# Kernel optimization log

Measured on AMD Instinct MI355X. Metric: run time of the kernel, lower is better.

Reference implementation:

```python
import jax, jax.numpy as jnp
import numpy as np

B, IN_C, L, D, K, DEPTH, OUT = 16, 3, 2048, 256, 8, 4, 1
F = L // 2 + 1
EPS = 1e-5


def _hilbert_basis_rfft(grid_size, k):
    # Hilbert matrix Z[i,j] = 1/(i+j+1), symmetric PSD; take top-k eigvecs.
    i = np.arange(grid_size, dtype=np.float64)
    Z = 1.0 / (i[:, None] + i[None, :] + 1.0)
    w, V = np.linalg.eigh(Z)
    idx = np.argsort(w)[::-1][:k]
    Vt = V.T[idx]                                   # (k, L)
    Phi_f = np.fft.rfft(Vt, n=grid_size, axis=-1)   # (k, L//2+1) complex
    return Phi_f.astype(np.complex64)


def setup_inputs() -> dict:
    key = jax.random.key(0)
    ks = jax.random.split(key, 10)
    phi = _hilbert_basis_rfft(L, K)
    s = 0.05
    return {
        "x": jax.random.normal(ks[0], (B, IN_C, L), jnp.float32),
        "lift_w": jax.random.normal(ks[1], (D, IN_C + 1), jnp.float32) * s,
        "lift_b": jax.random.normal(ks[2], (D,), jnp.float32) * s,
        "theta": jax.random.normal(ks[3], (DEPTH, K, D, D), jnp.float32) * (1.0 / np.sqrt(D)),
        "ln_gamma": jnp.ones((DEPTH, D), jnp.float32),
        "ln_beta": jnp.zeros((DEPTH, D), jnp.float32),
        "glu_val_w": jax.random.normal(ks[4], (DEPTH, D, D), jnp.float32) * (1.0 / np.sqrt(D)),
        "glu_val_b": jax.random.normal(ks[5], (DEPTH, D), jnp.float32) * s,
        "glu_gate_w": jax.random.normal(ks[6], (DEPTH, D, D), jnp.float32) * (1.0 / np.sqrt(D)),
        "glu_gate_b": jax.random.normal(ks[7], (DEPTH, D), jnp.float32) * s,
        "head_w": jax.random.normal(ks[8], (OUT, D), jnp.float32) * (1.0 / np.sqrt(D)),
        "head_b": jax.random.normal(ks[9], (OUT,), jnp.float32) * s,
        "phi_real": jnp.asarray(phi.real, jnp.float32),
        "phi_imag": jnp.asarray(phi.imag, jnp.float32),
    }


def _layernorm_channels(h, gamma, beta):
    # h: (b, d, t); normalize over channel dim d (matches LayerNorm on transposed input)
    mu = jnp.mean(h, axis=1, keepdims=True)
    var = jnp.mean(jnp.square(h - mu), axis=1, keepdims=True)
    z = (h - mu) * jax.lax.rsqrt(var + EPS)
    return z * gamma[None, :, None] + beta[None, :, None]


def reference(x, lift_w, lift_b, theta, ln_gamma, ln_beta,
              glu_val_w, glu_val_b, glu_gate_w, glu_gate_b,
              head_w, head_b, phi_real, phi_imag):
    phi = phi_real + 1j * phi_imag                      # (K, F) complex
    phi_c = jnp.conj(phi)
    # add grid coordinate channel
    coords = jnp.linspace(0.0, 1.0, L, dtype=x.dtype)
    coords = jnp.broadcast_to(coords[None, None, :], (x.shape[0], 1, L))
    h = jnp.concatenate([x, coords], axis=1)            # (b, in+1, L)
    # pointwise lift (Conv1d kernel_size=1, norm=Identity)
    h = jnp.einsum("oi,bit->bot", lift_w, h) + lift_b[None, :, None]
    for i in range(DEPTH):
        z = _layernorm_channels(h, ln_gamma[i], ln_beta[i])
        Xf = jnp.fft.rfft(z, axis=-1)                   # (b, d, F) complex64
        # Exploit FFT linearity: S = sum_{l,d} Theta[l,h,d] * irfft(Xf[b,d] * conj(Phi[l]))
        #                          = irfft( sum_{l,d} Theta[l,h,d]*conj(Phi[l,f]) * Xf[b,d,f] )
        W = jnp.einsum("lhd,lf->hdf", theta[i].astype(Xf.dtype), phi_c)  # (h, d, F)
        Sf = jnp.einsum("bdf,hdf->bhf", Xf, W)          # (b, h, F)
        S = jnp.fft.irfft(Sf, n=L, axis=-1)             # (b, h, L)
        V = jnp.einsum("od,bdt->bot", glu_val_w[i], S) + glu_val_b[i][None, :, None]
        G = jax.nn.sigmoid(jnp.einsum("od,bdt->bot", glu_gate_w[i], S) + glu_gate_b[i][None, :, None])
        h = h + V * G                                   # residual + GLU
    y = jnp.einsum("od,bdt->bot", head_w, h) + head_b[None, :, None]
    return y
```

## Files before the change

kernel.cpp:

```cpp
#include <hip/hip_runtime.h>
#include <math.h>

#define NB 16
#define CIN 3
#define LL 2048
#define DD 256
#define KK 8
#define NDEPTH 4
#define FF 1025
#define FFP 1032
#define LOGL 11

typedef _Float16 half8 __attribute__((ext_vector_type(8)));
typedef float f32x4 __attribute__((ext_vector_type(4)));

union H8 { half8 h8; unsigned int u[4]; uint4 q; };
union H2 { _Float16 h[2]; unsigned int u; };

__device__ inline float2 cmul(const float2 a, const float2 b){
    return make_float2(a.x*b.x - a.y*b.y, a.x*b.y + a.y*b.x);
}

__global__ void twiddle_kernel(float2* __restrict__ tw){
    int j = blockIdx.x*blockDim.x + threadIdx.x;
    if (j < LL/2){
        double ang = -2.0*3.14159265358979323846*(double)j/(double)LL;
        tw[j] = make_float2((float)cos(ang), (float)sin(ang));
    }
}

__global__ void conv_w_kernel(const float* __restrict__ wv, const float* __restrict__ wg,
                              _Float16* __restrict__ Wf){
    int idx = blockIdx.x*256 + threadIdx.x;
    int layer = idx >> 17;
    int vg = (idx >> 16) & 1;
    int rem = idx & 65535;
    int o = rem >> 8, d = rem & 255;
    const float* src = (vg ? wg : wv) + ((size_t)layer << 16);
    float val = src[(o << 8) + d];
    size_t dst = ((((size_t)(layer*2+vg)*16 + (o>>4))*8 + (d>>5))*64
                  + (o&15) + 16*((d>>3)&3))*8 + (d&7);
    Wf[dst] = (_Float16)val;
}

__global__ void transpose_theta_kernel(const float* __restrict__ in, float* __restrict__ out){
    __shared__ float tile[32][33];
    int m = blockIdx.z;
    int c0 = blockIdx.x*32, r0 = blockIdx.y*32;
    int tx = threadIdx.x & 31, ty = threadIdx.x >> 5;
    const float* src = in + (size_t)m*DD*DD;
    float* dst = out + (size_t)m*DD*DD;
    #pragma unroll
    for (int i = 0; i < 4; ++i){
        tile[ty + i*8][tx] = src[(size_t)(r0 + ty + i*8)*DD + c0 + tx];
    }
    __syncthreads();
    #pragma unroll
    for (int i = 0; i < 4; ++i){
        dst[(size_t)(c0 + ty + i*8)*DD + r0 + tx] = tile[tx][ty + i*8];
    }
}

__global__ __launch_bounds__(256) void lift_ln_kernel(const float* __restrict__ x,
        const float* __restrict__ lw, const float* __restrict__ lb,
        const float* __restrict__ gamma, const float* __restrict__ beta,
        float* __restrict__ h, float* __restrict__ z){
    __shared__ float red[2][4][64];
    __shared__ float stat[2][64];
    __shared__ float gb[512];
    int tid = threadIdx.x;
    int t = tid & 63, dg = tid >> 6;
    int b = blockIdx.y;
    int tg = blockIdx.x*64 + t;
    gb[tid] = gamma[tid];
    gb[256 + tid] = beta[tid];
    const float* xb = x + (size_t)b*CIN*LL;
    float x0 = xb[tg], x1 = xb[LL + tg], x2 = xb[2*LL + tg];
    float coord = (float)tg * (1.0f/(LL-1));
    float hv[64];
    float s = 0.f, ss = 0.f;
    float* hp = h + (size_t)b*DD*LL + tg;
    #pragma unroll
    for (int j = 0; j < 64; ++j){
        int d = dg*64 + j;
        float4 w = *(const float4*)&lw[d*4];
        float v = lb[d];
        v = fmaf(w.x, x0, v); v = fmaf(w.y, x1, v);
        v = fmaf(w.z, x2, v); v = fmaf(w.w, coord, v);
        hv[j] = v;
        s += v; ss = fmaf(v, v, ss);
        hp[(size_t)d*LL] = v;
    }
    red[0][dg][t] = s; red[1][dg][t] = ss;
    __syncthreads();
    if (tid < 64){
        float S1 = red[0][0][tid] + red[0][1][tid] + red[0][2][tid] + red[0][3][tid];
        float S2 = red[1][0][tid] + red[1][1][tid] + red[1][2][tid] + red[1][3][tid];
        float mu = S1*(1.0f/DD);
        float var = S2*(1.0f/DD) - mu*mu;
        stat[0][tid] = mu;
        stat[1][tid] = rsqrtf(var + 1e-5f);
    }
    __syncthreads();
    float mu = stat[0][t], rs = stat[1][t];
    float* zp = z + (size_t)b*DD*LL + tg;
    #pragma unroll
    for (int j = 0; j < 64; ++j){
        int d = dg*64 + j;
        zp[(size_t)d*LL] = (hv[j] - mu)*rs*gb[d] + gb[256 + d];
    }
}

__global__ __launch_bounds__(256) void fft_fwd_pair_kernel(const float* __restrict__ in,
                                                           unsigned int* __restrict__ XfH,
                                                           const float2* __restrict__ tw){
    __shared__ float2 a[LL];
    int blk = blockIdx.x;
    const float* src0 = in + (size_t)(blk*2)*LL;
    const float* src1 = src0 + LL;
    int tid = threadIdx.x;
    #pragma unroll
    for (int i = 0; i < LL/256; ++i){
        int idx = tid + i*256;
        int rev = __brev((unsigned)idx) >> (32-LOGL);
        a[rev] = make_float2(src0[idx], src1[idx]);
    }
    __syncthreads();
    for (int s = 0; s < LOGL; ++s){
        int half = 1 << s;
        #pragma unroll
        for (int jj = 0; jj < 4; ++jj){
            int j = tid + jj*256;
            int grp = j >> s;
            int pos = j & (half-1);
            int i1 = (grp << (s+1)) + pos;
            int i2 = i1 + half;
            float2 w = tw[pos << (LOGL-1-s)];
            float2 u = a[i1];
            float2 v = cmul(w, a[i2]);
            a[i1] = make_float2(u.x+v.x, u.y+v.y);
            a[i2] = make_float2(u.x-v.x, u.y-v.y);
        }
        __syncthreads();
    }
    unsigned int* dst0 = XfH + (size_t)(blk*2)*FFP;
    unsigned int* dst1 = dst0 + FFP;
    #pragma unroll
    for (int i = 0; i < 5; ++i){
        int f = tid + i*256;
        if (f <= 1024){
            int m = (LL - f) & (LL-1);
            float2 A = a[f], B = a[m];
            H2 p0, p1;
            p0.h[0] = (_Float16)(0.5f*(A.x + B.x));
            p0.h[1] = (_Float16)(0.5f*(A.y - B.y));
            p1.h[0] = (_Float16)(0.5f*(A.y + B.y));
            p1.h[1] = (_Float16)(0.5f*(B.x - A.x));
            dst0[f] = p0.u;
            dst1[f] = p1.u;
        }
    }
}

__global__ __launch_bounds__(256) void fft_inv_pair_kernel(const float2* __restrict__ in,
                                                           unsigned int* __restrict__ Sfrag,
                                                           const float2* __restrict__ tw){
    __shared__ float2 a[LL];
    int blk = blockIdx.x;
    const float2* src0 = in + (size_t)(blk*2)*FF;
    const float2* src1 = src0 + FF;
    int tid = threadIdx.x;
    #pragma unroll
    for (int i = 0; i < LL/256; ++i){
        int idx = tid + i*256;
        float2 Y;
        if (idx <= 1024){
            float2 s0 = src0[idx], s1 = src1[idx];
            Y = make_float2(s0.x - s1.y, s0.y + s1.x);
        } else {
            int m = LL - idx;
            float2 s0 = src0[m], s1 = src1[m];
            Y = make_float2(s0.x + s1.y, s1.x - s0.y);
        }
        int rev = __brev((unsigned)idx) >> (32-LOGL);
        a[rev] = Y;
    }
    __syncthreads();
    for (int s = 0; s < LOGL; ++s){
        int half = 1 << s;
        #pragma unroll
        for (int jj = 0; jj < 4; ++jj){
            int j = tid + jj*256;
            int grp = j >> s;
            int pos = j & (half-1);
            int i1 = (grp << (s+1)) + pos;
            int i2 = i1 + half;
            float2 w = tw[pos << (LOGL-1-s)];
            w.y = -w.y;
            float2 u = a[i1];
            float2 v = cmul(w, a[i2]);
            a[i1] = make_float2(u.x+v.x, u.y+v.y);
            a[i2] = make_float2(u.x-v.x, u.y-v.y);
        }
        __syncthreads();
    }
    int b = blk >> 7, dl = (blk & 127)*2;
    int kc = dl >> 5, lq4 = (dl >> 3) & 3, jh = (dl & 7) >> 1;
    unsigned int* dst = Sfrag + ((size_t)(b*8 + kc)*128)*64*4;
    const float sc = 1.0f/(float)LL;
    #pragma unroll
    for (int i = 0; i < LL/256; ++i){
        int t = tid + i*256;
        float2 v = a[t];
        H2 p;
        p.h[0] = (_Float16)(v.x*sc);
        p.h[1] = (_Float16)(v.y*sc);
        dst[(((t>>4)*64) + (t&15) + 16*lq4)*4 + jh] = p.u;
    }
}

__global__ __launch_bounds__(256, 2) void spectral3_kernel(
    const unsigned int* __restrict__ XfH,
    const float* __restrict__ thetaT,
    const float* __restrict__ phr, const float* __restrict__ phim,
    float2* __restrict__ Sf){
    __shared__ unsigned int Apairs[8*64*8];
    __shared__ float2 phi_s[8*KK];
    int tid = threadIdx.x;
    int w = tid >> 6, lane = tid & 63;
    int n = lane & 15, kp = lane >> 4;
    int f0 = blockIdx.x * 8;
    int h0 = blockIdx.y * 64;
    int h = h0 + w*16 + n;

    if (tid < 64){
        int ff = tid >> 3, l = tid & 7;
        phi_s[tid] = make_float2(phr[l*FF + f0 + ff], -phim[l*FF + f0 + ff]);
    }

    f32x4 accre[8], accim[8];
    #pragma unroll
    for (int i = 0; i < 8; ++i){
        accre[i] = (f32x4){0.f,0.f,0.f,0.f};
        accim[i] = (f32x4){0.f,0.f,0.f,0.f};
    }

    for (int kc = 0; kc < 8; ++kc){
        float th[8][8];
        #pragma unroll
        for (int l = 0; l < 8; ++l)
            #pragma unroll
            for (int j = 0; j < 8; ++j)
                th[l][j] = thetaT[((size_t)(l*DD) + kc*32 + kp*8 + j)*DD + h];

        __syncthreads();
        #pragma unroll
        for (int s = 0; s < 2; ++s){
            int b = tid & 15;
            int dd = s*16 + (tid >> 4);
            const uint4* src = (const uint4*)(XfH + ((size_t)(b*DD + kc*32 + dd)*FFP + f0));
            uint4 v0 = src[0], v1 = src[1];
            int L = b + 16*(dd >> 3), j = dd & 7;
            unsigned int vv[8] = {v0.x, v0.y, v0.z, v0.w, v1.x, v1.y, v1.z, v1.w};
            #pragma unroll
            for (int ff = 0; ff < 8; ++ff){
                int A = ff*2048 + L*32 + j*4;
                A ^= ((A >> 7) & 3) << 5;
                *(unsigned int*)((char*)Apairs + A) = vv[ff];
            }
        }
        __syncthreads();

        #pragma unroll
        for (int ff = 0; ff < 8; ++ff){
            float pr[8], pi[8];
            #pragma unroll
            for (int l = 0; l < 8; ++l){
                float2 p = phi_s[ff*8 + l];
                pr[l] = p.x; pi[l] = p.y;
            }
            int Ab = ff*2048 + lane*32;
            Ab ^= ((Ab >> 7) & 3) << 5;
            uint4 lo = *(const uint4*)((const char*)Apairs + Ab);
            uint4 hi = *(const uint4*)((const char*)Apairs + Ab + 16);
            unsigned int dw[8] = {lo.x, lo.y, lo.z, lo.w, hi.x, hi.y, hi.z, hi.w};
            H8 Are, Aim, Anim;
            #pragma unroll
            for (int k = 0; k < 4; ++k){
                Are.u[k]  = __builtin_amdgcn_perm(dw[2*k+1], dw[2*k], 0x05040100u);
                Aim.u[k]  = __builtin_amdgcn_perm(dw[2*k+1], dw[2*k], 0x07060302u);
                Anim.u[k] = Aim.u[k] ^ 0x80008000u;
            }
            float wre[8], wim[8];
            #pragma unroll
            for (int j = 0; j < 8; ++j){
                float re = 0.f, im = 0.f;
                #pragma unroll
                for (int l = 0; l < 8; ++l){
                    re = fmaf(th[l][j], pr[l], re);
                    im = fmaf(th[l][j], pi[l], im);
                }
                wre[j] = re; wim[j] = im;
            }
            H8 Bre, Bim;
            #pragma unroll
            for (int j = 0; j < 8; ++j){
                Bre.h8[j] = (_Float16)wre[j];
                Bim.h8[j] = (_Float16)wim[j];
            }
            accre[ff] = __builtin_amdgcn_mfma_f32_16x16x32_f16(Are.h8,  Bre.h8, accre[ff], 0, 0, 0);
            accre[ff] = __builtin_amdgcn_mfma_f32_16x16x32_f16(Anim.h8, Bim.h8, accre[ff], 0, 0, 0);
            accim[ff] = __builtin_amdgcn_mfma_f32_16x16x32_f16(Are.h8,  Bim.h8, accim[ff], 0, 0, 0);
            accim[ff] = __builtin_amdgcn_mfma_f32_16x16x32_f16(Aim.h8,  Bre.h8, accim[ff], 0, 0, 0);
        }
    }
    #pragma unroll
    for (int ff = 0; ff < 8; ++ff){
        #pragma unroll
        for (int r = 0; r < 4; ++r){
            int b = kp*4 + r;
            Sf[((size_t)(b*DD) + h)*FF + f0 + ff] = make_float2(accre[ff][r], accim[ff][r]);
        }
    }
}

__global__ __launch_bounds__(256) void nyq_kernel(const unsigned int* __restrict__ XfH,
    const float* __restrict__ thetaT,
    const float* __restrict__ phr, const float* __restrict__ phim,
    float2* __restrict__ Sf){
    __shared__ float2 red[256];
    int tid = threadIdx.x;
    int hb = blockIdx.x, b = blockIdx.y;
    int h = hb*16 + (tid & 15);
    int dp = tid >> 4;
    float pr[KK], pi[KK];
    #pragma unroll
    for (int l = 0; l < KK; ++l){ pr[l] = phr[l*FF + 1024]; pi[l] = -phim[l*FF + 1024]; }
    float2 acc = make_float2(0.f, 0.f);
    for (int j = 0; j < 16; ++j){
        int d = dp*16 + j;
        float wre = 0.f, wim = 0.f;
        #pragma unroll
        for (int l = 0; l < KK; ++l){
            float t = thetaT[((size_t)l*DD + d)*DD + h];
            wre = fmaf(t, pr[l], wre);
            wim = fmaf(t, pi[l], wim);
        }
        H2 u; u.u = XfH[(size_t)(b*DD + d)*FFP + 1024];
        float2 x = make_float2((float)u.h[0], (float)u.h[1]);
        acc.x = fmaf(x.x, wre, fmaf(-x.y, wim, acc.x));
        acc.y = fmaf(x.x, wim, fmaf( x.y, wre, acc.y));
    }
    red[tid] = acc;
    __syncthreads();
    if (tid < 16){
        float2 s = make_float2(0.f, 0.f);
        #pragma unroll
        for (int k = 0; k < 16; ++k){ s.x += red[tid + k*16].x; s.y += red[tid + k*16].y; }
        Sf[((size_t)b*DD + hb*16 + tid)*FF + 1024] = s;
    }
}

template<int MODE>
__global__ __launch_bounds__(256, 2) void glu_mfma_kernel(
    const uint4* __restrict__ Sfrag,
    const uint4* __restrict__ WfL,
    const float* __restrict__ bv, const float* __restrict__ bg,
    float* __restrict__ h, float* __restrict__ outp,
    const float* __restrict__ aux1, const float* __restrict__ aux2){
    __shared__ float sb[1024];
    __shared__ float red[2][4][4][16];
    __shared__ float stat[2][4][16];
    int tid = threadIdx.x;
    int w = tid >> 6, lane = tid & 63;
    int tl = lane & 15, lq = lane >> 4;
    int b = blockIdx.y, tb4 = blockIdx.x;

    sb[tid] = bv[tid];
    sb[256 + tid] = bg[tid];
    sb[512 + tid] = aux1[tid];
    if (MODE == 0) sb[768 + tid] = aux2[tid];
    __syncthreads();

    f32x4 aV[4][4], aG[4][4];
    #pragma unroll
    for (int mt = 0; mt < 4; ++mt)
        #pragma unroll
        for (int nt = 0; nt < 4; ++nt){
            aV[mt][nt] = (f32x4){0.f,0.f,0.f,0.f};
            aG[mt][nt] = (f32x4){0.f,0.f,0.f,0.f};
        }

    for (int kc = 0; kc < 8; ++kc){
        H8 Bf[4];
        #pragma unroll
        for (int nt = 0; nt < 4; ++nt)
            Bf[nt].q = Sfrag[((size_t)(b*8 + kc)*128 + tb4*4 + nt)*64 + lane];
        H8 Av[4], Ag[4];
        #pragma unroll
        for (int mt = 0; mt < 4; ++mt){
            int ot = w*4 + mt;
            Av[mt].q = WfL[((size_t)(ot)*8 + kc)*64 + lane];
            Ag[mt].q = WfL[((size_t)(16 + ot)*8 + kc)*64 + lane];
        }
        #pragma unroll
        for (int mt = 0; mt < 4; ++mt)
            #pragma unroll
            for (int nt = 0; nt < 4; ++nt){
                aV[mt][nt] = __builtin_amdgcn_mfma_f32_16x16x32_f16(Av[mt].h8, Bf[nt].h8, aV[mt][nt], 0, 0, 0);
                aG[mt][nt] = __builtin_amdgcn_mfma_f32_16x16x32_f16(Ag[mt].h8, Bf[nt].h8, aG[mt][nt], 0, 0, 0);
            }
    }

    #pragma unroll
    for (int mt = 0; mt < 4; ++mt){
        #pragma unroll
        for (int r = 0; r < 4; ++r){
            int o = w*64 + mt*16 + lq*4 + r;
            float bvv = sb[o], bgv = sb[256 + o];
            float* hp = h + ((size_t)(b*DD + o))*LL + tb4*64 + tl;
            #pragma unroll
            for (int nt = 0; nt < 4; ++nt){
                float v = aV[mt][nt][r] + bvv;
                float g = aG[mt][nt][r] + bgv;
                g = 1.0f/(1.0f + __expf(-g));
                float cur = hp[nt*16] + v*g;
                if (MODE == 0) hp[nt*16] = cur;
                aV[mt][nt][r] = cur;
            }
        }
    }

    float s[4], ss[4];
    #pragma unroll
    for (int nt = 0; nt < 4; ++nt){ s[nt] = 0.f; ss[nt] = 0.f; }
    #pragma unroll
    for (int mt = 0; mt < 4; ++mt)
        #pragma unroll
        for (int r = 0; r < 4; ++r){
            int o = w*64 + mt*16 + lq*4 + r;
            float wo = (MODE == 0) ? 1.0f : sb[512 + o];
            #pragma unroll
            for (int nt = 0; nt < 4; ++nt){
                float cur = aV[mt][nt][r];
                if (MODE == 0){ s[nt] += cur; ss[nt] = fmaf(cur, cur, ss[nt]); }
                else { s[nt] = fmaf(wo, cur, s[nt]); }
            }
        }
    #pragma unroll
    for (int nt = 0; nt < 4; ++nt){
        s[nt] += __shfl_xor(s[nt], 16); s[nt] += __shfl_xor(s[nt], 32);
        if (MODE == 0){ ss[nt] += __shfl_xor(ss[nt], 16); ss[nt] += __shfl_xor(ss[nt], 32); }
    }
    if (lq == 0){
        #pragma unroll
        for (int nt = 0; nt < 4; ++nt){
            red[0][w][nt][tl] = s[nt];
            if (MODE == 0) red[1][w][nt][tl] = ss[nt];
        }
    }
    __syncthreads();
    if (MODE == 0){
        if (tid < 64){
            int nt = tid >> 4, t2 = tid & 15;
            float S1 = red[0][0][nt][t2] + red[0][1][nt][t2] + red[0][2][nt][t2] + red[0][3][nt][t2];
            float S2 = red[1][0][nt][t2] + red[1][1][nt][t2] + red[1][2][nt][t2] + red[1][3][nt][t2];
            float mu = S1*(1.0f/DD);
            float var = S2*(1.0f/DD) - mu*mu;
            stat[0][nt][t2] = mu;
            stat[1][nt][t2] = rsqrtf(var + 1e-5f);
        }
        __syncthreads();
        #pragma unroll
        for (int mt = 0; mt < 4; ++mt){
            #pragma unroll
            for (int r = 0; r < 4; ++r){
                int o = w*64 + mt*16 + lq*4 + r;
                float gam = sb[512 + o], bet = sb[768 + o];
                float* zp = outp + ((size_t)(b*DD + o))*LL + tb4*64 + tl;
                #pragma unroll
                for (int nt = 0; nt < 4; ++nt){
                    float zv = (aV[mt][nt][r] - stat[0][nt][tl])*stat[1][nt][tl]*gam + bet;
                    zp[nt*16] = zv;
                }
            }
        }
    } else {
        if (tid < 64){
            int nt = tid >> 4, t2 = tid & 15;
            float S1 = red[0][0][nt][t2] + red[0][1][nt][t2] + red[0][2][nt][t2] + red[0][3][nt][t2];
            outp[(size_t)b*LL + tb4*64 + tid] = S1 + aux2[0];
        }
    }
}

extern "C" void kernel_launch(void* const* d_in, const int* in_sizes, int n_in,
                              void* d_out, int out_size, void* d_ws, size_t ws_size,
                              hipStream_t stream){
    (void)in_sizes; (void)n_in; (void)out_size; (void)ws_size;
    const float* x      = (const float*)d_in[0];
    const float* lift_w = (const float*)d_in[1];
    const float* lift_b = (const float*)d_in[2];
    const float* theta  = (const float*)d_in[3];
    const float* ln_g   = (const float*)d_in[4];
    const float* ln_b   = (const float*)d_in[5];
    const float* gvw    = (const float*)d_in[6];
    const float* gvb    = (const float*)d_in[7];
    const float* ggw    = (const float*)d_in[8];
    const float* ggb    = (const float*)d_in[9];
    const float* hw     = (const float*)d_in[10];
    const float* hb     = (const float*)d_in[11];
    const float* phr    = (const float*)d_in[12];
    const float* phim   = (const float*)d_in[13];
    float* out = (float*)d_out;

    char* ws = (char*)d_ws;
    size_t off = 0;
    float2* tw  = (float2*)(ws + off); off += (size_t)(LL/2)*sizeof(float2);
    _Float16* Wf = (_Float16*)(ws + off); off += (size_t)NDEPTH*2*DD*DD*2;
    float*  thT = (float*)(ws + off);  off += (size_t)NDEPTH*KK*DD*DD*4;
    off = (off + 255) & ~(size_t)255;
    float*  h   = (float*)(ws + off);  off += (size_t)NB*DD*LL*4;
    float*  z   = (float*)(ws + off);  off += (size_t)NB*DD*LL*4;
    unsigned int* XfH = (unsigned int*)(ws + off); off += (size_t)NB*DD*FFP*4;
    unsigned int* Sfrag = XfH;
    off = (off + 255) & ~(size_t)255;
    float2* Sf  = (float2*)(ws + off); off += (size_t)NB*DD*FF*8;

    twiddle_kernel<<<4, 256, 0, stream>>>(tw);
    conv_w_kernel<<<(NDEPTH*2*DD*DD)/256, 256, 0, stream>>>(gvw, ggw, Wf);
    transpose_theta_kernel<<<dim3(8,8,NDEPTH*KK), 256, 0, stream>>>(theta, thT);
    lift_ln_kernel<<<dim3(LL/64, NB), 256, 0, stream>>>(x, lift_w, lift_b, ln_g, ln_b, h, z);

    for (int layer = 0; layer < NDEPTH; ++layer){
        const float* thL = thT + (size_t)layer*KK*DD*DD;
        const uint4* WfL = (const uint4*)(Wf + (size_t)layer*2*DD*DD);
        fft_fwd_pair_kernel<<<NB*DD/2, 256, 0, stream>>>(z, XfH, tw);
        spectral3_kernel<<<dim3(128,4), 256, 0, stream>>>(XfH, thL, phr, phim, Sf);
        nyq_kernel<<<dim3(16,16), 256, 0, stream>>>(XfH, thL, phr, phim, Sf);
        fft_inv_pair_kernel<<<NB*DD/2, 256, 0, stream>>>(Sf, Sfrag, tw);
        if (layer < NDEPTH-1){
            glu_mfma_kernel<0><<<dim3(LL/64, NB), 256, 0, stream>>>(
                (const uint4*)Sfrag, WfL,
                gvb + layer*DD, ggb + layer*DD, h, z,
                ln_g + (layer+1)*DD, ln_b + (layer+1)*DD);
        } else {
            glu_mfma_kernel<1><<<dim3(LL/64, NB), 256, 0, stream>>>(
                (const uint4*)Sfrag, WfL,
                gvb + layer*DD, ggb + layer*DD, h, out, hw, hb);
        }
    }
}
```

Measured before the change: 604.6 us.

## Use radix-4 FFT stages and split spectral work across more blocks

The forward and inverse FFT kernels now use fused radix-4 passes (five of them) plus one final radix-2 pass, replacing eleven radix-2 passes. This cuts the number of shared-memory round trips and barriers per transform. The spectral kernel now has each wave handle 4 frequencies for 16 output channels instead of 8 frequencies for 64 channels. It launches twice as many blocks with a higher occupancy hint, but the shared A tile and the theta loads are now repeated in more blocks.

```diff
diff --git a/kernel.cpp b/kernel.cpp
--- a/kernel.cpp
+++ b/kernel.cpp
@@ -126,23 +126,43 @@
         a[rev] = make_float2(src0[idx], src1[idx]);
     }
     __syncthreads();
-    for (int s = 0; s < LOGL; ++s){
-        int half = 1 << s;
-        #pragma unroll
-        for (int jj = 0; jj < 4; ++jj){
-            int j = tid + jj*256;
-            int grp = j >> s;
-            int pos = j & (half-1);
-            int i1 = (grp << (s+1)) + pos;
-            int i2 = i1 + half;
-            float2 w = tw[pos << (LOGL-1-s)];
-            float2 u = a[i1];
-            float2 v = cmul(w, a[i2]);
-            a[i1] = make_float2(u.x+v.x, u.y+v.y);
-            a[i2] = make_float2(u.x-v.x, u.y-v.y);
+    #pragma unroll
+    for (int sp = 0; sp < 5; ++sp){
+        const int s = sp*2;
+        const int hs = 1 << s;
+        #pragma unroll
+        for (int gg = 0; gg < 2; ++gg){
+            int g = tid + gg*256;
+            int pos = g & (hs-1);
+            int grp = g >> s;
+            int q = (grp << (s+2)) + pos;
+            float2 ws = tw[pos << (LOGL-1-s)];
+            float2 w1 = tw[pos << (LOGL-2-s)];
+            float2 w2 = tw[(pos+hs) << (LOGL-2-s)];
+            float2 a0 = a[q], a1 = a[q+hs], a2 = a[q+2*hs], a3 = a[q+3*hs];
+            float2 t1 = cmul(ws, a1), t3 = cmul(ws, a3);
+            float2 x0 = make_float2(a0.x+t1.x, a0.y+t1.y);
+            float2 x1 = make_float2(a0.x-t1.x, a0.y-t1.y);
+            float2 x2 = make_float2(a2.x+t3.x, a2.y+t3.y);
+            float2 x3 = make_float2(a2.x-t3.x, a2.y-t3.y);
+            float2 u1 = cmul(w1, x2), u2 = cmul(w2, x3);
+            a[q]       = make_float2(x0.x+u1.x, x0.y+u1.y);
+            a[q+2*hs]  = make_float2(x0.x-u1.x, x0.y-u1.y);
+            a[q+hs]    = make_float2(x1.x+u2.x, x1.y+u2.y);
+            a[q+3*hs]  = make_float2(x1.x-u2.x, x1.y-u2.y);
         }
         __syncthreads();
     }
+    #pragma unroll
+    for (int jj = 0; jj < 4; ++jj){
+        int j = tid + jj*256;
+        float2 w = tw[j];
+        float2 u = a[j];
+        float2 v = cmul(w, a[j+1024]);
+        a[j]      = make_float2(u.x+v.x, u.y+v.y);
+        a[j+1024] = make_float2(u.x-v.x, u.y-v.y);
+    }
+    __syncthreads();
     unsigned int* dst0 = XfH + (size_t)(blk*2)*FFP;
     unsigned int* dst1 = dst0 + FFP;
     #pragma unroll
@@ -186,24 +206,43 @@
         a[rev] = Y;
     }
     __syncthreads();
-    for (int s = 0; s < LOGL; ++s){
-        int half = 1 << s;
-        #pragma unroll
-        for (int jj = 0; jj < 4; ++jj){
-            int j = tid + jj*256;
-            int grp = j >> s;
-            int pos = j & (half-1);
-            int i1 = (grp << (s+1)) + pos;
-            int i2 = i1 + half;
-            float2 w = tw[pos << (LOGL-1-s)];
-            w.y = -w.y;
-            float2 u = a[i1];
-            float2 v = cmul(w, a[i2]);
-            a[i1] = make_float2(u.x+v.x, u.y+v.y);
-            a[i2] = make_float2(u.x-v.x, u.y-v.y);
+    #pragma unroll
+    for (int sp = 0; sp < 5; ++sp){
+        const int s = sp*2;
+        const int hs = 1 << s;
+        #pragma unroll
+        for (int gg = 0; gg < 2; ++gg){
+            int g = tid + gg*256;
+            int pos = g & (hs-1);
+            int grp = g >> s;
+            int q = (grp << (s+2)) + pos;
+            float2 ws = tw[pos << (LOGL-1-s)];  ws.y = -ws.y;
+            float2 w1 = tw[pos << (LOGL-2-s)];  w1.y = -w1.y;
+            float2 w2 = tw[(pos+hs) << (LOGL-2-s)]; w2.y = -w2.y;
+            float2 a0 = a[q], a1 = a[q+hs], a2 = a[q+2*hs], a3 = a[q+3*hs];
+            float2 t1 = cmul(ws, a1), t3 = cmul(ws, a3);
+            float2 x0 = make_float2(a0.x+t1.x, a0.y+t1.y);
+            float2 x1 = make_float2(a0.x-t1.x, a0.y-t1.y);
+            float2 x2 = make_float2(a2.x+t3.x, a2.y+t3.y);
+            float2 x3 = make_float2(a2.x-t3.x, a2.y-t3.y);
+            float2 u1 = cmul(w1, x2), u2 = cmul(w2, x3);
+            a[q]       = make_float2(x0.x+u1.x, x0.y+u1.y);
+            a[q+2*hs]  = make_float2(x0.x-u1.x, x0.y-u1.y);
+            a[q+hs]    = make_float2(x1.x+u2.x, x1.y+u2.y);
+            a[q+3*hs]  = make_float2(x1.x-u2.x, x1.y-u2.y);
         }
         __syncthreads();
     }
+    #pragma unroll
+    for (int jj = 0; jj < 4; ++jj){
+        int j = tid + jj*256;
+        float2 w = tw[j]; w.y = -w.y;
+        float2 u = a[j];
+        float2 v = cmul(w, a[j+1024]);
+        a[j]      = make_float2(u.x+v.x, u.y+v.y);
+        a[j+1024] = make_float2(u.x-v.x, u.y-v.y);
+    }
+    __syncthreads();
     int b = blk >> 7, dl = (blk & 127)*2;
     int kc = dl >> 5, lq4 = (dl >> 3) & 3, jh = (dl & 7) >> 1;
     unsigned int* dst = Sfrag + ((size_t)(b*8 + kc)*128)*64*4;
@@ -219,7 +258,7 @@
     }
 }
 
-__global__ __launch_bounds__(256, 2) void spectral3_kernel(
+__global__ __launch_bounds__(256, 3) void spectral4_kernel(
     const unsigned int* __restrict__ XfH,
     const float* __restrict__ thetaT,
     const float* __restrict__ phr, const float* __restrict__ phim,
@@ -229,18 +268,20 @@
     int tid = threadIdx.x;
     int w = tid >> 6, lane = tid & 63;
     int n = lane & 15, kp = lane >> 4;
+    int ffb = (w >> 1) * 4;
+    int hh = w & 1;
     int f0 = blockIdx.x * 8;
-    int h0 = blockIdx.y * 64;
-    int h = h0 + w*16 + n;
+    int h0 = blockIdx.y * 32;
+    int h = h0 + hh*16 + n;
 
     if (tid < 64){
         int ff = tid >> 3, l = tid & 7;
         phi_s[tid] = make_float2(phr[l*FF + f0 + ff], -phim[l*FF + f0 + ff]);
     }
 
-    f32x4 accre[8], accim[8];
-    #pragma unroll
-    for (int i = 0; i < 8; ++i){
+    f32x4 accre[4], accim[4];
+    #pragma unroll
+    for (int i = 0; i < 4; ++i){
         accre[i] = (f32x4){0.f,0.f,0.f,0.f};
         accim[i] = (f32x4){0.f,0.f,0.f,0.f};
     }
@@ -272,7 +313,8 @@
         __syncthreads();
 
         #pragma unroll
-        for (int ff = 0; ff < 8; ++ff){
+        for (int ffl = 0; ffl < 4; ++ffl){
+            int ff = ffb + ffl;
             float pr[8], pi[8];
             #pragma unroll
             for (int l = 0; l < 8; ++l){
@@ -308,18 +350,18 @@
                 Bre.h8[j] = (_Float16)wre[j];
                 Bim.h8[j] = (_Float16)wim[j];
             }
-            accre[ff] = __builtin_amdgcn_mfma_f32_16x16x32_f16(Are.h8,  Bre.h8, accre[ff], 0, 0, 0);
-            accre[ff] = __builtin_amdgcn_mfma_f32_16x16x32_f16(Anim.h8, Bim.h8, accre[ff], 0, 0, 0);
-            accim[ff] = __builtin_amdgcn_mfma_f32_16x16x32_f16(Are.h8,  Bim.h8, accim[ff], 0, 0, 0);
-            accim[ff] = __builtin_amdgcn_mfma_f32_16x16x32_f16(Aim.h8,  Bre.h8, accim[ff], 0, 0, 0);
-        }
-    }
-    #pragma unroll
-    for (int ff = 0; ff < 8; ++ff){
+            accre[ffl] = __builtin_amdgcn_mfma_f32_16x16x32_f16(Are.h8,  Bre.h8, accre[ffl], 0, 0, 0);
+            accre[ffl] = __builtin_amdgcn_mfma_f32_16x16x32_f16(Anim.h8, Bim.h8, accre[ffl], 0, 0, 0);
+            accim[ffl] = __builtin_amdgcn_mfma_f32_16x16x32_f16(Are.h8,  Bim.h8, accim[ffl], 0, 0, 0);
+            accim[ffl] = __builtin_amdgcn_mfma_f32_16x16x32_f16(Aim.h8,  Bre.h8, accim[ffl], 0, 0, 0);
+        }
+    }
+    #pragma unroll
+    for (int ffl = 0; ffl < 4; ++ffl){
         #pragma unroll
         for (int r = 0; r < 4; ++r){
             int b = kp*4 + r;
-            Sf[((size_t)(b*DD) + h)*FF + f0 + ff] = make_float2(accre[ff][r], accim[ff][r]);
+            Sf[((size_t)(b*DD) + h)*FF + f0 + ffb + ffl] = make_float2(accre[ffl][r], accim[ffl][r]);
         }
     }
 }
@@ -536,7 +578,7 @@
         const float* thL = thT + (size_t)layer*KK*DD*DD;
         const uint4* WfL = (const uint4*)(Wf + (size_t)layer*2*DD*DD);
         fft_fwd_pair_kernel<<<NB*DD/2, 256, 0, stream>>>(z, XfH, tw);
-        spectral3_kernel<<<dim3(128,4), 256, 0, stream>>>(XfH, thL, phr, phim, Sf);
+        spectral4_kernel<<<dim3(128,8), 256, 0, stream>>>(XfH, thL, phr, phim, Sf);
         nyq_kernel<<<dim3(16,16), 256, 0, stream>>>(XfH, thL, phr, phim, Sf);
         fft_inv_pair_kernel<<<NB*DD/2, 256, 0, stream>>>(Sf, Sfrag, tw);
         if (layer < NDEPTH-1){
```

New measurement: 667.3 us. 1.1x slower.
